# Kernel optimization log

Hardware: AMD Instinct MI355X
Metric: run time of the kernel (lower is better)

Reference implementation:

```python
import jax, jax.numpy as jnp
import numpy as np

STEP_SIZE = 0.005   # ray-march step length in normalized [-1,1] coords
RES = 128           # occupancy grid resolution per axis
NUM_BATCH = 4       # number of conditioned batches (B)
N_RAYS = 32768


def setup_inputs() -> dict:
    key = jax.random.key(0)
    k1, k2, k3, k4 = jax.random.split(key, 4)
    rays_o = jax.random.uniform(k1, (N_RAYS, 3), dtype=jnp.float32, minval=-0.5, maxval=0.5)
    d = jax.random.normal(k2, (N_RAYS, 3), dtype=jnp.float32)
    rays_d = d / jnp.linalg.norm(d, axis=-1, keepdims=True)
    rays_bidx = jax.random.randint(k3, (N_RAYS,), 0, NUM_BATCH)
    occ_grid = jax.random.uniform(k4, (NUM_BATCH, RES, RES, RES)) > 0.5
    return {"occ_grid": occ_grid, "rays_o": rays_o, "rays_d": rays_d,
            "rays_bidx": rays_bidx, "max_steps": 512}


def reference(occ_grid, rays_o, rays_d, rays_bidx, max_steps):
    """Batched occupancy-grid ray marching (uniform steps, dt_gamma=0, perturb=False).

    Returns:
      pts  [N, S, 3]: sample positions, zeroed where not occupied/out of range
      t    [N, S]   : per-step ray parameter
      mask [N, S]   : bool, sample is inside box AND its voxel is occupied
    """
    eps = 1e-10
    # --- ray / AABB([-1,1]^3) intersection -> near/far per ray ---
    safe_d = jnp.where(jnp.abs(rays_d) < eps,
                       jnp.where(rays_d >= 0, eps, -eps), rays_d)
    inv_d = 1.0 / safe_d
    t0 = (-1.0 - rays_o) * inv_d
    t1 = (1.0 - rays_o) * inv_d
    tmin = jnp.max(jnp.minimum(t0, t1), axis=-1)   # [N]
    tmax = jnp.min(jnp.maximum(t0, t1), axis=-1)   # [N]
    near = jnp.maximum(tmin, 0.0)

    # --- uniform marching: t_i = near + (i + 0.5) * step ---
    steps = jnp.arange(max_steps, dtype=rays_o.dtype)            # [S]
    t = near[:, None] + (steps + 0.5) * STEP_SIZE                # [N, S]
    pts = rays_o[:, None, :] + t[..., None] * rays_d[:, None, :]  # [N, S, 3]
    in_box = (t < tmax[:, None]) & (tmax > near)[:, None]        # [N, S]

    # --- occupancy query: gidx = clamp(((p/2+0.5)*R).long(), 0, R-1) ---
    gidx = jnp.clip(((pts * 0.5 + 0.5) * RES).astype(jnp.int32), 0, RES - 1)
    occ = occ_grid[rays_bidx[:, None], gidx[..., 0], gidx[..., 1], gidx[..., 2]]  # [N, S]
    mask = occ & in_box

    out_pts = pts * mask[..., None].astype(pts.dtype)
    return out_pts, t, mask
```

## Files before the change

### kernel.cpp

```cpp
#include <hip/hip_runtime.h>

constexpr int RESI   = 128;
constexpr int NSTEPS = 512;

__global__ __launch_bounds__(128) void occ_march_kernel(
    const int*   __restrict__ occ,
    const float* __restrict__ rays_o,
    const float* __restrict__ rays_d,
    const int*   __restrict__ rays_bidx,
    float*       __restrict__ out_pts,
    float*       __restrict__ out_t,
    float*       __restrict__ out_mask,
    int n_rays)
{
#pragma clang fp contract(off)
    const int ray = blockIdx.x;
    if (ray >= n_rays) return;

    const float ox = rays_o[3 * ray + 0];
    const float oy = rays_o[3 * ray + 1];
    const float oz = rays_o[3 * ray + 2];
    const float dx = rays_d[3 * ray + 0];
    const float dy = rays_d[3 * ray + 1];
    const float dz = rays_d[3 * ray + 2];
    const int   b  = rays_bidx[ray];

    const float eps = 1e-10f;
    const float sdx = (fabsf(dx) < eps) ? ((dx >= 0.0f) ? eps : -eps) : dx;
    const float sdy = (fabsf(dy) < eps) ? ((dy >= 0.0f) ? eps : -eps) : dy;
    const float sdz = (fabsf(dz) < eps) ? ((dz >= 0.0f) ? eps : -eps) : dz;
    const float invx = 1.0f / sdx;
    const float invy = 1.0f / sdy;
    const float invz = 1.0f / sdz;

    const float t0x = (-1.0f - ox) * invx;
    const float t1x = ( 1.0f - ox) * invx;
    const float t0y = (-1.0f - oy) * invy;
    const float t1y = ( 1.0f - oy) * invy;
    const float t0z = (-1.0f - oz) * invz;
    const float t1z = ( 1.0f - oz) * invz;

    const float tmin = fmaxf(fmaxf(fminf(t0x, t1x), fminf(t0y, t1y)), fminf(t0z, t1z));
    const float tmax = fminf(fminf(fmaxf(t0x, t1x), fmaxf(t0y, t1y)), fmaxf(t0z, t1z));
    const float nearv  = fmaxf(tmin, 0.0f);
    const bool  ray_ok = (tmax > nearv);

    const int* __restrict__ g = occ + (size_t)b * (RESI * RESI * RESI);

    const int s0 = (int)threadIdx.x * 4;

    float tv[4], mv[4], p[12];

#pragma unroll
    for (int i = 0; i < 4; ++i) {
        const int   s  = s0 + i;
        const float ts = nearv + ((float)s + 0.5f) * 0.005f;
        const float px = ox + ts * dx;
        const float py = oy + ts * dy;
        const float pz = oz + ts * dz;

        const bool in_box = ray_ok && (ts < tmax);

        int gx = (int)((px * 0.5f + 0.5f) * 128.0f);
        int gy = (int)((py * 0.5f + 0.5f) * 128.0f);
        int gz = (int)((pz * 0.5f + 0.5f) * 128.0f);
        gx = min(max(gx, 0), RESI - 1);
        gy = min(max(gy, 0), RESI - 1);
        gz = min(max(gz, 0), RESI - 1);

        const int  o = g[(gx * RESI + gy) * RESI + gz];
        const bool m = in_box && (o != 0);

        tv[i] = ts;
        mv[i] = m ? 1.0f : 0.0f;
        p[3 * i + 0] = m ? px : 0.0f;
        p[3 * i + 1] = m ? py : 0.0f;
        p[3 * i + 2] = m ? pz : 0.0f;
    }

    const size_t base = (size_t)ray * NSTEPS + (size_t)s0;

    *(float4*)(out_t    + base) = make_float4(tv[0], tv[1], tv[2], tv[3]);
    *(float4*)(out_mask + base) = make_float4(mv[0], mv[1], mv[2], mv[3]);

    float4* pp = (float4*)(out_pts + base * 3);
    pp[0] = make_float4(p[0], p[1], p[2],  p[3]);
    pp[1] = make_float4(p[4], p[5], p[6],  p[7]);
    pp[2] = make_float4(p[8], p[9], p[10], p[11]);
}

extern "C" void kernel_launch(void* const* d_in, const int* in_sizes, int n_in,
                              void* d_out, int out_size, void* d_ws, size_t ws_size,
                              hipStream_t stream) {
    const int*   occ    = (const int*)  d_in[0];
    const float* rays_o = (const float*)d_in[1];
    const float* rays_d = (const float*)d_in[2];
    const int*   bidx   = (const int*)  d_in[3];

    const int n_rays = in_sizes[3];

    float* out      = (float*)d_out;
    float* out_pts  = out;
    float* out_t    = out + (size_t)n_rays * NSTEPS * 3;
    float* out_mask = out_t + (size_t)n_rays * NSTEPS;

    occ_march_kernel<<<n_rays, 128, 0, stream>>>(occ, rays_o, rays_d, bidx,
                                                 out_pts, out_t, out_mask, n_rays);
}
```

Before: 415.6 us.

## Pack occupancy grid into tiled 8x8x8 bitfield and skip lookups outside box

Adds a pre-pass kernel that packs the int32 occupancy grid into a bitfield laid out as 8x8x8 voxel bricks, 32 bits per word. The march kernel then reads one word and tests a bit, instead of gathering an int32 per sample. It also skips the grid lookup for samples outside the box. The aim is to shrink the gathered working set to fit in cache and improve spatial locality, at the cost of an extra launch and a full pass over the 32 MB grid on every call.

```diff
diff --git a/kernel.cpp b/kernel.cpp
--- a/kernel.cpp
+++ b/kernel.cpp
@@ -2,9 +2,38 @@
 
 constexpr int RESI   = 128;
 constexpr int NSTEPS = 512;
+constexpr int GRID_WORDS_PER_BATCH = 65536;
+
+__global__ __launch_bounds__(256) void occ_pack_tiled_kernel(
+    const int* __restrict__ occ, unsigned int* __restrict__ bits)
+{
+    const int w = blockIdx.x * blockDim.x + threadIdx.x;
+    const int b   = w >> 16;
+    const int rem = w & 65535;
+    const int blockid = rem >> 4;
+    const int wib     = rem & 15;
+    const int bx = blockid >> 8;
+    const int by = (blockid >> 4) & 15;
+    const int bz = blockid & 15;
+    const int gx  = bx * 8 + (wib >> 1);
+    const int gy0 = by * 8 + (wib & 1) * 4;
+    const int gz0 = bz * 8;
+
+    const int* __restrict__ src = occ + (((size_t)b * RESI + gx) * RESI + gy0) * RESI + gz0;
+
+    unsigned int word = 0;
+#pragma unroll
+    for (int a = 0; a < 4; ++a) {
+        const int* row = src + a * RESI;
+#pragma unroll
+        for (int c = 0; c < 8; ++c)
+            word |= (row[c] != 0 ? 1u : 0u) << (a * 8 + c);
+    }
+    bits[w] = word;
+}
 
 __global__ __launch_bounds__(128) void occ_march_kernel(
-    const int*   __restrict__ occ,
+    const unsigned int* __restrict__ gridbits,
     const float* __restrict__ rays_o,
     const float* __restrict__ rays_d,
     const int*   __restrict__ rays_bidx,
@@ -45,7 +74,7 @@
     const float nearv  = fmaxf(tmin, 0.0f);
     const bool  ray_ok = (tmax > nearv);
 
-    const int* __restrict__ g = occ + (size_t)b * (RESI * RESI * RESI);
+    const unsigned int* __restrict__ gb = gridbits + (size_t)b * GRID_WORDS_PER_BATCH;
 
     const int s0 = (int)threadIdx.x * 4;
 
@@ -61,15 +90,23 @@
 
         const bool in_box = ray_ok && (ts < tmax);
 
-        int gx = (int)((px * 0.5f + 0.5f) * 128.0f);
-        int gy = (int)((py * 0.5f + 0.5f) * 128.0f);
-        int gz = (int)((pz * 0.5f + 0.5f) * 128.0f);
-        gx = min(max(gx, 0), RESI - 1);
-        gy = min(max(gy, 0), RESI - 1);
-        gz = min(max(gz, 0), RESI - 1);
+        bool m = false;
+        if (in_box) {
+            int gx = (int)((px * 0.5f + 0.5f) * 128.0f);
+            int gy = (int)((py * 0.5f + 0.5f) * 128.0f);
+            int gz = (int)((pz * 0.5f + 0.5f) * 128.0f);
+            gx = min(max(gx, 0), RESI - 1);
+            gy = min(max(gy, 0), RESI - 1);
+            gz = min(max(gz, 0), RESI - 1);
 
-        const int  o = g[(gx * RESI + gy) * RESI + gz];
-        const bool m = in_box && (o != 0);
+            const unsigned int blockid = ((unsigned)(gx >> 3) << 8) |
+                                         ((unsigned)(gy >> 3) << 4) |
+                                          (unsigned)(gz >> 3);
+            const unsigned int wib    = (((unsigned)gx & 7u) << 1) | (((unsigned)gy >> 2) & 1u);
+            const unsigned int word   = gb[(blockid << 4) | wib];
+            const unsigned int bitpos = (((unsigned)gy & 3u) << 3) | ((unsigned)gz & 7u);
+            m = (word >> bitpos) & 1u;
+        }
 
         tv[i] = ts;
         mv[i] = m ? 1.0f : 0.0f;
@@ -98,12 +135,17 @@
     const int*   bidx   = (const int*)  d_in[3];
 
     const int n_rays = in_sizes[3];
+    const int n_vox  = in_sizes[0];
+    const int n_words = n_vox / 32;
 
     float* out      = (float*)d_out;
     float* out_pts  = out;
     float* out_t    = out + (size_t)n_rays * NSTEPS * 3;
     float* out_mask = out_t + (size_t)n_rays * NSTEPS;
 
-    occ_march_kernel<<<n_rays, 128, 0, stream>>>(occ, rays_o, rays_d, bidx,
+    unsigned int* bits = (unsigned int*)d_ws;
+
+    occ_pack_tiled_kernel<<<n_words / 256, 256, 0, stream>>>(occ, bits);
+    occ_march_kernel<<<n_rays, 128, 0, stream>>>(bits, rays_o, rays_d, bidx,
                                                  out_pts, out_t, out_mask, n_rays);
 }
```

Result: faster. 362.0 us (-12.9%).
